# Performance work log

Hardware: AMD Instinct MI355X
Metric: run time of the kernel (lower is better)

Reference implementation:

```python
import jax, jax.numpy as jnp
import numpy as np

INPUT_DIM = 3
NUM_LEVELS = 16
LEVEL_DIM = 2
PER_LEVEL_SCALE = 2
BASE_RES = 16
MAX_PARAMS = 2 ** 19
BATCH = 2 ** 21

PRIMES = np.array([1, 2654435761, 805459861], dtype=np.uint32)
SORTED_BIN_MASK = np.triu(np.ones((INPUT_DIM + 1, INPUT_DIM), dtype=np.int32))


def _offsets():
    offs, off = [], 0
    for i in range(NUM_LEVELS):
        res = int(np.ceil(BASE_RES * PER_LEVEL_SCALE ** i))
        p = min(MAX_PARAMS, res ** INPUT_DIM)
        p = int(np.ceil(p / 32) * 32)
        off += p
        offs.append(off)
    return offs

OFFSETS = _offsets()  # cumulative, last entry = total table rows = 7114752


def setup_inputs() -> dict:
    key = jax.random.key(0)
    k1, k2 = jax.random.split(key)
    inputs = jax.random.uniform(k1, (BATCH, INPUT_DIM), dtype=jnp.float32)
    # xavier-uniform-ish init for the hash table
    total = OFFSETS[-1]
    a = float(np.sqrt(6.0 / (total + LEVEL_DIM)))
    embeddings = jax.random.uniform(k2, (total, LEVEL_DIM), dtype=jnp.float32,
                                    minval=-a, maxval=a)
    return {"inputs": inputs, "embeddings": embeddings}


def _fast_hash(ind_u32, hash_size):
    # ind_u32: [..., 3] uint32; uint32 multiply wraps mod 2^32 == (& 0xFFFFFFFF)
    h = ind_u32 * jnp.asarray(PRIMES)
    h = h[..., 0] ^ h[..., 1] ^ h[..., 2]
    return h % jnp.uint32(hash_size)


def _forward(inputs, embeddings):
    bin_mask_tbl = jnp.asarray(SORTED_BIN_MASK)  # [d+1, d]
    outs = []
    prev = 0
    for i in range(NUM_LEVELS):
        res = int(np.ceil(BASE_RES * PER_LEVEL_SCALE ** i))
        x = inputs * res                      # [B, d]
        xi = x.astype(jnp.int32)              # trunc == floor for x >= 0
        xf = x - jax.lax.stop_gradient(xi.astype(x.dtype))
        inds = jnp.argsort(xf, axis=-1)
        sorted_xf = jnp.take_along_axis(xf, inds, axis=-1)
        inv_inds = jnp.argsort(inds, axis=-1)
        bin_mask = bin_mask_tbl[:, inv_inds].transpose(1, 0, 2)  # [B, d+1, d]
        neigs = xi[:, None, :] + bin_mask                        # [B, d+1, d]
        hash_size = OFFSETS[i] - prev
        hids = _fast_hash(neigs.astype(jnp.uint32), hash_size).astype(jnp.int32) + prev
        feats = embeddings[hids]              # [B, d+1, level_dim] irregular gather
        # barycentric-style weights: consecutive diffs of sorted fracs padded with 0/1
        w_upper = jnp.concatenate([sorted_xf, jnp.ones_like(sorted_xf[..., :1])], axis=-1)
        w_lower = jnp.concatenate([jnp.zeros_like(sorted_xf[..., :1]), sorted_xf], axis=-1)
        w = (w_upper - w_lower)[..., None]    # [B, d+1, 1]
        outs.append(jnp.sum(feats * w, axis=-2))  # [B, level_dim]
        prev = OFFSETS[i]
    return jnp.concatenate(outs, axis=-1)     # [B, num_levels * level_dim]


def reference(inputs, embeddings):
    return _forward(inputs, embeddings)
```

## Files before the change

kernel.cpp:

```cpp
#include <hip/hip_runtime.h>
#include <hip/hip_fp16.h>
#include <stdint.h>


constexpr uint32_t kBatch   = 1u << 21;
constexpr size_t   kWsNeed  = (size_t)kBatch * 16u * sizeof(uint32_t);

typedef float f32x2 __attribute__((ext_vector_type(2)));
typedef float f32x4 __attribute__((ext_vector_type(4)));

constexpr uint32_t PREV[16] = {
    0u, 4096u, 36864u, 299008u, 823296u, 1347584u, 1871872u, 2396160u,
    2920448u, 3444736u, 3969024u, 4493312u, 5017600u, 5541888u, 6066176u, 6590464u};
constexpr uint32_t MASK[16] = {
    4095u, 32767u, 262143u, 524287u, 524287u, 524287u, 524287u, 524287u,
    524287u, 524287u, 524287u, 524287u, 524287u, 524287u, 524287u, 524287u};

__device__ __forceinline__ void corner_hashes_weights(
    float x0, float x1, float x2, float res, uint32_t mask, uint32_t prev,
    uint32_t& g0, uint32_t& g1, uint32_t& g2, uint32_t& g3,
    float& sa, float& sb, float& sc)
{
    const float fx0 = x0 * res;
    const float fx1 = x1 * res;
    const float fx2 = x2 * res;
    const int i0 = (int)fx0;
    const int i1 = (int)fx1;
    const int i2 = (int)fx2;
    const float f0 = fx0 - (float)i0;
    const float f1 = fx1 - (float)i1;
    const float f2 = fx2 - (float)i2;

    const int r0 = (int)(f1 < f0) + (int)(f2 < f0);
    const int r1 = (int)(f0 < f1) + (int)(f2 < f1) + (int)(f0 == f1);
    const int r2 = (int)(f0 < f2) + (int)(f1 < f2) + (int)(f0 == f2) + (int)(f1 == f2);

    sa = fminf(fminf(f0, f1), f2);
    sc = fmaxf(fmaxf(f0, f1), f2);
    sb = __builtin_amdgcn_fmed3f(f0, f1, f2);

    const uint32_t A0 = (uint32_t)i0;
    const uint32_t A1 = A0 + 1u;
    const uint32_t B0 = (uint32_t)i1 * 2654435761u;
    const uint32_t B1 = ((uint32_t)i1 + 1u) * 2654435761u;
    const uint32_t C0 = (uint32_t)i2 * 805459861u;
    const uint32_t C1 = ((uint32_t)i2 + 1u) * 805459861u;

    const uint32_t h0 = A1 ^ B1 ^ C1;
    const uint32_t h1 = (r0 >= 1 ? A1 : A0) ^ (r1 >= 1 ? B1 : B0) ^ (r2 >= 1 ? C1 : C0);
    const uint32_t h2 = (r0 >= 2 ? A1 : A0) ^ (r1 >= 2 ? B1 : B0) ^ (r2 >= 2 ? C1 : C0);
    const uint32_t h3 = A0 ^ B0 ^ C0;

    g0 = (h0 & mask) + prev;
    g1 = (h1 & mask) + prev;
    g2 = (h2 & mask) + prev;
    g3 = (h3 & mask) + prev;
}

__device__ __forceinline__ uint32_t pack_f16x2(float x, float y) {
    const __half hx = __float2half(x);
    const __half hy = __float2half(y);
    return (uint32_t)__half_as_ushort(hx) | ((uint32_t)__half_as_ushort(hy) << 16);
}

__device__ __forceinline__ float lo_h(uint32_t p) {
    return __half2float(__ushort_as_half((unsigned short)(p & 0xFFFFu)));
}
__device__ __forceinline__ float hi_h(uint32_t p) {
    return __half2float(__ushort_as_half((unsigned short)(p >> 16)));
}


__global__ __launch_bounds__(1024) void hybrid012(
    const float* __restrict__ in,
    const float* __restrict__ emb,
    uint32_t* __restrict__ scr)
{
    __shared__ uint32_t t0[4096];
    __shared__ uint32_t t1[32768];

    const uint32_t t = threadIdx.x;

#pragma unroll
    for (uint32_t i = 0u; i < 4u; ++i) {
        const uint32_t r = t + 1024u * i;
        const f32x2 v = *reinterpret_cast<const f32x2*>(emb + 2u * r);
        t0[r] = pack_f16x2(v.x, v.y);
    }
#pragma unroll
    for (uint32_t i = 0u; i < 32u; ++i) {
        const uint32_t r = t + 1024u * i;
        const f32x2 v = *reinterpret_cast<const f32x2*>(emb + 2u * (4096u + r));
        t1[r] = pack_f16x2(v.x, v.y);
    }
    __syncthreads();

    const uint32_t tid = blockIdx.x * 1024u + t;

#pragma unroll 1
    for (uint32_t k = 0u; k < 8u; ++k) {
        const uint32_t b = tid + k * 262144u;
        const float x0 = __builtin_nontemporal_load(in + 3u * b + 0u);
        const float x1 = __builtin_nontemporal_load(in + 3u * b + 1u);
        const float x2 = __builtin_nontemporal_load(in + 3u * b + 2u);

        uint32_t g0, g1, g2, g3;
        float sa2, sb2, sc2;
        corner_hashes_weights(x0, x1, x2, 64.0f, 262143u, 36864u,
                              g0, g1, g2, g3, sa2, sb2, sc2);
        f32x2 e2a = *reinterpret_cast<const f32x2*>(emb + 2u * g0);
        f32x2 e2b = *reinterpret_cast<const f32x2*>(emb + 2u * g1);
        f32x2 e2c = *reinterpret_cast<const f32x2*>(emb + 2u * g2);
        f32x2 e2d = *reinterpret_cast<const f32x2*>(emb + 2u * g3);

        {
            uint32_t l0, l1, l2, l3;
            float sa, sb, sc;
            corner_hashes_weights(x0, x1, x2, 16.0f, 4095u, 0u,
                                  l0, l1, l2, l3, sa, sb, sc);
            const uint32_t p0 = t0[l0], p1 = t0[l1], p2 = t0[l2], p3 = t0[l3];
            const float w0 = sa, w1 = sb - sa, w2 = sc - sb, w3 = 1.0f - sc;
            const float vx = w0 * lo_h(p0) + w1 * lo_h(p1) + w2 * lo_h(p2) + w3 * lo_h(p3);
            const float vy = w0 * hi_h(p0) + w1 * hi_h(p1) + w2 * hi_h(p2) + w3 * hi_h(p3);
            __builtin_nontemporal_store(pack_f16x2(vx, vy), scr + b);
        }
        {
            uint32_t l0, l1, l2, l3;
            float sa, sb, sc;
            corner_hashes_weights(x0, x1, x2, 32.0f, 32767u, 0u,
                                  l0, l1, l2, l3, sa, sb, sc);
            const uint32_t p0 = t1[l0], p1 = t1[l1], p2 = t1[l2], p3 = t1[l3];
            const float w0 = sa, w1 = sb - sa, w2 = sc - sb, w3 = 1.0f - sc;
            const float vx = w0 * lo_h(p0) + w1 * lo_h(p1) + w2 * lo_h(p2) + w3 * lo_h(p3);
            const float vy = w0 * hi_h(p0) + w1 * hi_h(p1) + w2 * hi_h(p2) + w3 * hi_h(p3);
            __builtin_nontemporal_store(pack_f16x2(vx, vy), scr + (size_t)kBatch + b);
        }

        asm volatile("" : "+v"(e2a), "+v"(e2b), "+v"(e2c), "+v"(e2d));
        const float w0 = sa2, w1 = sb2 - sa2, w2 = sc2 - sb2, w3 = 1.0f - sc2;
        const float vx = w0 * e2a.x + w1 * e2b.x + w2 * e2c.x + w3 * e2d.x;
        const float vy = w0 * e2a.y + w1 * e2b.y + w2 * e2c.y + w3 * e2d.y;
        __builtin_nontemporal_store(pack_f16x2(vx, vy), scr + (size_t)2u * kBatch + b);
    }
}


__global__ __launch_bounds__(256) void gather13(
    const float* __restrict__ in,
    const float* __restrict__ emb,
    uint32_t* __restrict__ scr)
{
    const uint32_t bid  = blockIdx.x;
    const uint32_t lvl  = 3u + (bid >> 11);
    const uint32_t tid  = (bid & 2047u) * 256u + threadIdx.x;
    const uint32_t quarter = kBatch / 4u;

    const float res = (float)(16u << lvl);
    const uint32_t mask = MASK[lvl];
    const uint32_t prev = PREV[lvl];
    uint32_t* slab = scr + (size_t)lvl * kBatch;

    f32x2 e[4][4];
    float sa[4], sb[4], sc[4];

#pragma unroll
    for (int k = 0; k < 4; ++k) {
        const uint32_t b = tid + (uint32_t)k * quarter;
        const float x0 = __builtin_nontemporal_load(in + 3u * b + 0u);
        const float x1 = __builtin_nontemporal_load(in + 3u * b + 1u);
        const float x2 = __builtin_nontemporal_load(in + 3u * b + 2u);
        uint32_t g0, g1, g2, g3;
        corner_hashes_weights(x0, x1, x2, res, mask, prev, g0, g1, g2, g3,
                              sa[k], sb[k], sc[k]);
        e[k][0] = *reinterpret_cast<const f32x2*>(emb + 2u * g0);
        e[k][1] = *reinterpret_cast<const f32x2*>(emb + 2u * g1);
        e[k][2] = *reinterpret_cast<const f32x2*>(emb + 2u * g2);
        e[k][3] = *reinterpret_cast<const f32x2*>(emb + 2u * g3);
    }

    asm volatile(""
        : "+v"(e[0][0]), "+v"(e[0][1]), "+v"(e[0][2]), "+v"(e[0][3]),
          "+v"(e[1][0]), "+v"(e[1][1]), "+v"(e[1][2]), "+v"(e[1][3]),
          "+v"(e[2][0]), "+v"(e[2][1]), "+v"(e[2][2]), "+v"(e[2][3]),
          "+v"(e[3][0]), "+v"(e[3][1]), "+v"(e[3][2]), "+v"(e[3][3]));

#pragma unroll
    for (int k = 0; k < 4; ++k) {
        const float w0 = sa[k];
        const float w1 = sb[k] - sa[k];
        const float w2 = sc[k] - sb[k];
        const float w3 = 1.0f - sc[k];
        const float vx = w0 * e[k][0].x + w1 * e[k][1].x + w2 * e[k][2].x + w3 * e[k][3].x;
        const float vy = w0 * e[k][0].y + w1 * e[k][1].y + w2 * e[k][2].y + w3 * e[k][3].y;
        const uint32_t b = tid + (uint32_t)k * quarter;
        __builtin_nontemporal_store(pack_f16x2(vx, vy), slab + b);
    }
}

__global__ __launch_bounds__(256) void transpose16(
    const uint32_t* __restrict__ scr,
    float* __restrict__ out)
{
    const uint32_t b = blockIdx.x * 256u + threadIdx.x;

    uint32_t p[16];
#pragma unroll
    for (int l = 0; l < 16; ++l)
        p[l] = __builtin_nontemporal_load(scr + (size_t)l * kBatch + b);

    float* o = out + (size_t)b * 32u;
#pragma unroll
    for (int q = 0; q < 8; ++q) {
        f32x4 t;
        t.x = lo_h(p[2 * q + 0]);
        t.y = hi_h(p[2 * q + 0]);
        t.z = lo_h(p[2 * q + 1]);
        t.w = hi_h(p[2 * q + 1]);
        *reinterpret_cast<f32x4*>(o + 4 * q) = t;
    }
}


__global__ __launch_bounds__(256) void pyramid_fwd_mono(
    const float* __restrict__ in,
    const float* __restrict__ emb,
    float* __restrict__ out)
{
    const uint32_t b = blockIdx.x * 256u + threadIdx.x;
    const float x0 = in[3u * b + 0u];
    const float x1 = in[3u * b + 1u];
    const float x2 = in[3u * b + 2u];

#pragma unroll
    for (int g = 0; g < 2; ++g) {
        float o8[16];
#pragma unroll
        for (int k = 0; k < 8; ++k) {
            const int lvl = g * 8 + k;
            const float res = (float)(16 << lvl);
            uint32_t g0, g1, g2, g3;
            float sa, sb, sc;
            corner_hashes_weights(x0, x1, x2, res, MASK[lvl], PREV[lvl],
                                  g0, g1, g2, g3, sa, sb, sc);
            const f32x2 e0 = *reinterpret_cast<const f32x2*>(emb + 2u * g0);
            const f32x2 e1 = *reinterpret_cast<const f32x2*>(emb + 2u * g1);
            const f32x2 e2 = *reinterpret_cast<const f32x2*>(emb + 2u * g2);
            const f32x2 e3 = *reinterpret_cast<const f32x2*>(emb + 2u * g3);
            const float w0 = sa, w1 = sb - sa, w2 = sc - sb, w3 = 1.0f - sc;
            o8[2 * k + 0] = w0 * e0.x + w1 * e1.x + w2 * e2.x + w3 * e3.x;
            o8[2 * k + 1] = w0 * e0.y + w1 * e1.y + w2 * e2.y + w3 * e3.y;
        }
        f32x4* o = reinterpret_cast<f32x4*>(out + (size_t)b * 32u + (size_t)g * 16u);
#pragma unroll
        for (int q = 0; q < 4; ++q) {
            f32x4 v;
            v.x = o8[4 * q + 0];
            v.y = o8[4 * q + 1];
            v.z = o8[4 * q + 2];
            v.w = o8[4 * q + 3];
            o[q] = v;
        }
    }
}


extern "C" void kernel_launch(void* const* d_in, const int* in_sizes, int n_in,
                              void* d_out, int out_size, void* d_ws, size_t ws_size,
                              hipStream_t stream) {
    const float* in  = (const float*)d_in[0];
    const float* emb = (const float*)d_in[1];
    float* out = (float*)d_out;

    if (ws_size >= kWsNeed) {
        uint32_t* scr = (uint32_t*)d_ws;
        hipLaunchKernelGGL(hybrid012, dim3(256u), dim3(1024u), 0, stream, in, emb, scr);
        hipLaunchKernelGGL(gather13, dim3(13u * 2048u), dim3(256u), 0, stream, in, emb, scr);
        hipLaunchKernelGGL(transpose16, dim3(kBatch / 256u), dim3(256u), 0, stream, scr, out);
    } else {
        hipLaunchKernelGGL(pyramid_fwd_mono, dim3(kBatch / 256u), dim3(256u), 0, stream,
                           in, emb, out);
    }
}
```

Before: 662.7 us.

## Merge LDS-level kernel and global gather kernel into one conveyor launch

```diff
diff --git a/kernel.cpp b/kernel.cpp
--- a/kernel.cpp
+++ b/kernel.cpp
@@ -4,6 +4,7 @@
 
 
 constexpr uint32_t kBatch   = 1u << 21;
+constexpr uint32_t kQuarter = kBatch / 4u;
 constexpr size_t   kWsNeed  = (size_t)kBatch * 16u * sizeof(uint32_t);
 
 typedef float f32x2 __attribute__((ext_vector_type(2)));
@@ -71,7 +72,7 @@
 }
 
 
-__global__ __launch_bounds__(1024) void hybrid012(
+__global__ __launch_bounds__(1024) void conveyor14(
     const float* __restrict__ in,
     const float* __restrict__ emb,
     uint32_t* __restrict__ scr)
@@ -79,121 +80,124 @@
     __shared__ uint32_t t0[4096];
     __shared__ uint32_t t1[32768];
 
-    const uint32_t t = threadIdx.x;
-
-#pragma unroll
-    for (uint32_t i = 0u; i < 4u; ++i) {
-        const uint32_t r = t + 1024u * i;
-        const f32x2 v = *reinterpret_cast<const f32x2*>(emb + 2u * r);
-        t0[r] = pack_f16x2(v.x, v.y);
-    }
-#pragma unroll
-    for (uint32_t i = 0u; i < 32u; ++i) {
-        const uint32_t r = t + 1024u * i;
-        const f32x2 v = *reinterpret_cast<const f32x2*>(emb + 2u * (4096u + r));
-        t1[r] = pack_f16x2(v.x, v.y);
-    }
-    __syncthreads();
-
-    const uint32_t tid = blockIdx.x * 1024u + t;
-
-#pragma unroll 1
-    for (uint32_t k = 0u; k < 8u; ++k) {
-        const uint32_t b = tid + k * 262144u;
-        const float x0 = __builtin_nontemporal_load(in + 3u * b + 0u);
-        const float x1 = __builtin_nontemporal_load(in + 3u * b + 1u);
-        const float x2 = __builtin_nontemporal_load(in + 3u * b + 2u);
-
-        uint32_t g0, g1, g2, g3;
-        float sa2, sb2, sc2;
-        corner_hashes_weights(x0, x1, x2, 64.0f, 262143u, 36864u,
-                              g0, g1, g2, g3, sa2, sb2, sc2);
-        f32x2 e2a = *reinterpret_cast<const f32x2*>(emb + 2u * g0);
-        f32x2 e2b = *reinterpret_cast<const f32x2*>(emb + 2u * g1);
-        f32x2 e2c = *reinterpret_cast<const f32x2*>(emb + 2u * g2);
-        f32x2 e2d = *reinterpret_cast<const f32x2*>(emb + 2u * g3);
-
-        {
-            uint32_t l0, l1, l2, l3;
-            float sa, sb, sc;
-            corner_hashes_weights(x0, x1, x2, 16.0f, 4095u, 0u,
-                                  l0, l1, l2, l3, sa, sb, sc);
-            const uint32_t p0 = t0[l0], p1 = t0[l1], p2 = t0[l2], p3 = t0[l3];
-            const float w0 = sa, w1 = sb - sa, w2 = sc - sb, w3 = 1.0f - sc;
-            const float vx = w0 * lo_h(p0) + w1 * lo_h(p1) + w2 * lo_h(p2) + w3 * lo_h(p3);
-            const float vy = w0 * hi_h(p0) + w1 * hi_h(p1) + w2 * hi_h(p2) + w3 * hi_h(p3);
-            __builtin_nontemporal_store(pack_f16x2(vx, vy), scr + b);
-        }
-        {
-            uint32_t l0, l1, l2, l3;
-            float sa, sb, sc;
-            corner_hashes_weights(x0, x1, x2, 32.0f, 32767u, 0u,
-                                  l0, l1, l2, l3, sa, sb, sc);
-            const uint32_t p0 = t1[l0], p1 = t1[l1], p2 = t1[l2], p3 = t1[l3];
-            const float w0 = sa, w1 = sb - sa, w2 = sc - sb, w3 = 1.0f - sc;
-            const float vx = w0 * lo_h(p0) + w1 * lo_h(p1) + w2 * lo_h(p2) + w3 * lo_h(p3);
-            const float vy = w0 * hi_h(p0) + w1 * hi_h(p1) + w2 * hi_h(p2) + w3 * hi_h(p3);
-            __builtin_nontemporal_store(pack_f16x2(vx, vy), scr + (size_t)kBatch + b);
-        }
-
-        asm volatile("" : "+v"(e2a), "+v"(e2b), "+v"(e2c), "+v"(e2d));
-        const float w0 = sa2, w1 = sb2 - sa2, w2 = sc2 - sb2, w3 = 1.0f - sc2;
-        const float vx = w0 * e2a.x + w1 * e2b.x + w2 * e2c.x + w3 * e2d.x;
-        const float vy = w0 * e2a.y + w1 * e2b.y + w2 * e2c.y + w3 * e2d.y;
-        __builtin_nontemporal_store(pack_f16x2(vx, vy), scr + (size_t)2u * kBatch + b);
-    }
-}
-
-
-__global__ __launch_bounds__(256) void gather13(
-    const float* __restrict__ in,
-    const float* __restrict__ emb,
-    uint32_t* __restrict__ scr)
-{
-    const uint32_t bid  = blockIdx.x;
-    const uint32_t lvl  = 3u + (bid >> 11);
-    const uint32_t tid  = (bid & 2047u) * 256u + threadIdx.x;
-    const uint32_t quarter = kBatch / 4u;
+    const uint32_t bid = blockIdx.x;
+    const uint32_t lvl = 2u + (bid >> 9);
+    const uint32_t tid = (bid & 511u) * 1024u + threadIdx.x;
 
     const float res = (float)(16u << lvl);
     const uint32_t mask = MASK[lvl];
     const uint32_t prev = PREV[lvl];
     uint32_t* slab = scr + (size_t)lvl * kBatch;
 
-    f32x2 e[4][4];
-    float sa[4], sb[4], sc[4];
-
-#pragma unroll
-    for (int k = 0; k < 4; ++k) {
-        const uint32_t b = tid + (uint32_t)k * quarter;
-        const float x0 = __builtin_nontemporal_load(in + 3u * b + 0u);
-        const float x1 = __builtin_nontemporal_load(in + 3u * b + 1u);
-        const float x2 = __builtin_nontemporal_load(in + 3u * b + 2u);
-        uint32_t g0, g1, g2, g3;
-        corner_hashes_weights(x0, x1, x2, res, mask, prev, g0, g1, g2, g3,
-                              sa[k], sb[k], sc[k]);
-        e[k][0] = *reinterpret_cast<const f32x2*>(emb + 2u * g0);
-        e[k][1] = *reinterpret_cast<const f32x2*>(emb + 2u * g1);
-        e[k][2] = *reinterpret_cast<const f32x2*>(emb + 2u * g2);
-        e[k][3] = *reinterpret_cast<const f32x2*>(emb + 2u * g3);
-    }
-
-    asm volatile(""
-        : "+v"(e[0][0]), "+v"(e[0][1]), "+v"(e[0][2]), "+v"(e[0][3]),
-          "+v"(e[1][0]), "+v"(e[1][1]), "+v"(e[1][2]), "+v"(e[1][3]),
-          "+v"(e[2][0]), "+v"(e[2][1]), "+v"(e[2][2]), "+v"(e[2][3]),
-          "+v"(e[3][0]), "+v"(e[3][1]), "+v"(e[3][2]), "+v"(e[3][3]));
-
-#pragma unroll
-    for (int k = 0; k < 4; ++k) {
-        const float w0 = sa[k];
-        const float w1 = sb[k] - sa[k];
-        const float w2 = sc[k] - sb[k];
-        const float w3 = 1.0f - sc[k];
-        const float vx = w0 * e[k][0].x + w1 * e[k][1].x + w2 * e[k][2].x + w3 * e[k][3].x;
-        const float vy = w0 * e[k][0].y + w1 * e[k][1].y + w2 * e[k][2].y + w3 * e[k][3].y;
-        const uint32_t b = tid + (uint32_t)k * quarter;
-        __builtin_nontemporal_store(pack_f16x2(vx, vy), slab + b);
+    if (lvl == 2u) {
+#pragma unroll
+        for (uint32_t i = 0u; i < 4u; ++i) {
+            const uint32_t r = threadIdx.x + 1024u * i;
+            const f32x2 v = *reinterpret_cast<const f32x2*>(emb + 2u * r);
+            t0[r] = pack_f16x2(v.x, v.y);
+        }
+#pragma unroll
+        for (uint32_t i = 0u; i < 32u; ++i) {
+            const uint32_t r = threadIdx.x + 1024u * i;
+            const f32x2 v = *reinterpret_cast<const f32x2*>(emb + 2u * (4096u + r));
+            t1[r] = pack_f16x2(v.x, v.y);
+        }
+        __syncthreads();
+
+        float xin[4][3];
+        f32x2 e[4][4];
+        float sa2[4], sb2[4], sc2[4];
+#pragma unroll
+        for (int k = 0; k < 4; ++k) {
+            const uint32_t b = tid + (uint32_t)k * kQuarter;
+            xin[k][0] = __builtin_nontemporal_load(in + 3u * b + 0u);
+            xin[k][1] = __builtin_nontemporal_load(in + 3u * b + 1u);
+            xin[k][2] = __builtin_nontemporal_load(in + 3u * b + 2u);
+            uint32_t g0, g1, g2, g3;
+            corner_hashes_weights(xin[k][0], xin[k][1], xin[k][2], res, mask, prev,
+                                  g0, g1, g2, g3, sa2[k], sb2[k], sc2[k]);
+            e[k][0] = *reinterpret_cast<const f32x2*>(emb + 2u * g0);
+            e[k][1] = *reinterpret_cast<const f32x2*>(emb + 2u * g1);
+            e[k][2] = *reinterpret_cast<const f32x2*>(emb + 2u * g2);
+            e[k][3] = *reinterpret_cast<const f32x2*>(emb + 2u * g3);
+        }
+
+#pragma unroll
+        for (int k = 0; k < 4; ++k) {
+            const uint32_t b = tid + (uint32_t)k * kQuarter;
+            {
+                uint32_t l0, l1, l2, l3;
+                float sa, sb, sc;
+                corner_hashes_weights(xin[k][0], xin[k][1], xin[k][2],
+                                      16.0f, 4095u, 0u, l0, l1, l2, l3, sa, sb, sc);
+                const uint32_t p0 = t0[l0], p1 = t0[l1], p2 = t0[l2], p3 = t0[l3];
+                const float w0 = sa, w1 = sb - sa, w2 = sc - sb, w3 = 1.0f - sc;
+                const float vx = w0 * lo_h(p0) + w1 * lo_h(p1) + w2 * lo_h(p2) + w3 * lo_h(p3);
+                const float vy = w0 * hi_h(p0) + w1 * hi_h(p1) + w2 * hi_h(p2) + w3 * hi_h(p3);
+                __builtin_nontemporal_store(pack_f16x2(vx, vy), scr + b);
+            }
+            {
+                uint32_t l0, l1, l2, l3;
+                float sa, sb, sc;
+                corner_hashes_weights(xin[k][0], xin[k][1], xin[k][2],
+                                      32.0f, 32767u, 0u, l0, l1, l2, l3, sa, sb, sc);
+                const uint32_t p0 = t1[l0], p1 = t1[l1], p2 = t1[l2], p3 = t1[l3];
+                const float w0 = sa, w1 = sb - sa, w2 = sc - sb, w3 = 1.0f - sc;
+                const float vx = w0 * lo_h(p0) + w1 * lo_h(p1) + w2 * lo_h(p2) + w3 * lo_h(p3);
+                const float vy = w0 * hi_h(p0) + w1 * hi_h(p1) + w2 * hi_h(p2) + w3 * hi_h(p3);
+                __builtin_nontemporal_store(pack_f16x2(vx, vy), scr + (size_t)kBatch + b);
+            }
+        }
+
+        asm volatile(""
+            : "+v"(e[0][0]), "+v"(e[0][1]), "+v"(e[0][2]), "+v"(e[0][3]),
+              "+v"(e[1][0]), "+v"(e[1][1]), "+v"(e[1][2]), "+v"(e[1][3]),
+              "+v"(e[2][0]), "+v"(e[2][1]), "+v"(e[2][2]), "+v"(e[2][3]),
+              "+v"(e[3][0]), "+v"(e[3][1]), "+v"(e[3][2]), "+v"(e[3][3]));
+#pragma unroll
+        for (int k = 0; k < 4; ++k) {
+            const float w0 = sa2[k];
+            const float w1 = sb2[k] - sa2[k];
+            const float w2 = sc2[k] - sb2[k];
+            const float w3 = 1.0f - sc2[k];
+            const float vx = w0 * e[k][0].x + w1 * e[k][1].x + w2 * e[k][2].x + w3 * e[k][3].x;
+            const float vy = w0 * e[k][0].y + w1 * e[k][1].y + w2 * e[k][2].y + w3 * e[k][3].y;
+            const uint32_t b = tid + (uint32_t)k * kQuarter;
+            __builtin_nontemporal_store(pack_f16x2(vx, vy), slab + b);
+        }
+    } else {
+        f32x2 e[4][4];
+        float sa[4], sb[4], sc[4];
+#pragma unroll
+        for (int k = 0; k < 4; ++k) {
+            const uint32_t b = tid + (uint32_t)k * kQuarter;
+            const float x0 = __builtin_nontemporal_load(in + 3u * b + 0u);
+            const float x1 = __builtin_nontemporal_load(in + 3u * b + 1u);
+            const float x2 = __builtin_nontemporal_load(in + 3u * b + 2u);
+            uint32_t g0, g1, g2, g3;
+            corner_hashes_weights(x0, x1, x2, res, mask, prev, g0, g1, g2, g3,
+                                  sa[k], sb[k], sc[k]);
+            e[k][0] = *reinterpret_cast<const f32x2*>(emb + 2u * g0);
+            e[k][1] = *reinterpret_cast<const f32x2*>(emb + 2u * g1);
+            e[k][2] = *reinterpret_cast<const f32x2*>(emb + 2u * g2);
+            e[k][3] = *reinterpret_cast<const f32x2*>(emb + 2u * g3);
+        }
+        asm volatile(""
+            : "+v"(e[0][0]), "+v"(e[0][1]), "+v"(e[0][2]), "+v"(e[0][3]),
+              "+v"(e[1][0]), "+v"(e[1][1]), "+v"(e[1][2]), "+v"(e[1][3]),
+              "+v"(e[2][0]), "+v"(e[2][1]), "+v"(e[2][2]), "+v"(e[2][3]),
+              "+v"(e[3][0]), "+v"(e[3][1]), "+v"(e[3][2]), "+v"(e[3][3]));
+#pragma unroll
+        for (int k = 0; k < 4; ++k) {
+            const float w0 = sa[k];
+            const float w1 = sb[k] - sa[k];
+            const float w2 = sc[k] - sb[k];
+            const float w3 = 1.0f - sc[k];
+            const float vx = w0 * e[k][0].x + w1 * e[k][1].x + w2 * e[k][2].x + w3 * e[k][3].x;
+            const float vy = w0 * e[k][0].y + w1 * e[k][1].y + w2 * e[k][2].y + w3 * e[k][3].y;
+            const uint32_t b = tid + (uint32_t)k * kQuarter;
+            __builtin_nontemporal_store(pack_f16x2(vx, vy), slab + b);
+        }
     }
 }
 
@@ -273,9 +277,10 @@
 
     if (ws_size >= kWsNeed) {
         uint32_t* scr = (uint32_t*)d_ws;
-        hipLaunchKernelGGL(hybrid012, dim3(256u), dim3(1024u), 0, stream, in, emb, scr);
-        hipLaunchKernelGGL(gather13, dim3(13u * 2048u), dim3(256u), 0, stream, in, emb, scr);
-        hipLaunchKernelGGL(transpose16, dim3(kBatch / 256u), dim3(256u), 0, stream, scr, out);
+        hipLaunchKernelGGL(conveyor14, dim3(14u * 512u), dim3(1024u), 0, stream,
+                           in, emb, scr);
+        hipLaunchKernelGGL(transpose16, dim3(kBatch / 256u), dim3(256u), 0, stream,
+                           scr, out);
     } else {
         hipLaunchKernelGGL(pyramid_fwd_mono, dim3(kBatch / 256u), dim3(256u), 0, stream,
                            in, emb, out);
```

Measured after the change: 668.8 us. About the same (+0.9%).

## Merge low-level shared-table kernel and high-level gather kernel into one launch

Applied to the files above, without the earlier changes.

```diff
diff --git a/kernel.cpp b/kernel.cpp
--- a/kernel.cpp
+++ b/kernel.cpp
@@ -4,6 +4,7 @@
 
 
 constexpr uint32_t kBatch   = 1u << 21;
+constexpr uint32_t kQuarter = kBatch / 4u;
 constexpr size_t   kWsNeed  = (size_t)kBatch * 16u * sizeof(uint32_t);
 
 typedef float f32x2 __attribute__((ext_vector_type(2)));
@@ -71,7 +72,7 @@
 }
 
 
-__global__ __launch_bounds__(1024) void hybrid012(
+__global__ __launch_bounds__(1024) void conveyor16(
     const float* __restrict__ in,
     const float* __restrict__ emb,
     uint32_t* __restrict__ scr)
@@ -79,121 +80,111 @@
     __shared__ uint32_t t0[4096];
     __shared__ uint32_t t1[32768];
 
-    const uint32_t t = threadIdx.x;
-
-#pragma unroll
-    for (uint32_t i = 0u; i < 4u; ++i) {
-        const uint32_t r = t + 1024u * i;
-        const f32x2 v = *reinterpret_cast<const f32x2*>(emb + 2u * r);
-        t0[r] = pack_f16x2(v.x, v.y);
-    }
-#pragma unroll
-    for (uint32_t i = 0u; i < 32u; ++i) {
-        const uint32_t r = t + 1024u * i;
-        const f32x2 v = *reinterpret_cast<const f32x2*>(emb + 2u * (4096u + r));
-        t1[r] = pack_f16x2(v.x, v.y);
-    }
-    __syncthreads();
-
-    const uint32_t tid = blockIdx.x * 1024u + t;
+    const uint32_t bid = blockIdx.x;
+
+    if (bid < 13u * 512u) {
+        const uint32_t lvl = 3u + (bid >> 9);
+        const uint32_t tid = (bid & 511u) * 1024u + threadIdx.x;
+
+        const float res = (float)(16u << lvl);
+        const uint32_t mask = MASK[lvl];
+        const uint32_t prev = PREV[lvl];
+        uint32_t* slab = scr + (size_t)lvl * kBatch;
+
+        f32x2 e[4][4];
+        float sa[4], sb[4], sc[4];
+#pragma unroll
+        for (int k = 0; k < 4; ++k) {
+            const uint32_t b = tid + (uint32_t)k * kQuarter;
+            const float x0 = __builtin_nontemporal_load(in + 3u * b + 0u);
+            const float x1 = __builtin_nontemporal_load(in + 3u * b + 1u);
+            const float x2 = __builtin_nontemporal_load(in + 3u * b + 2u);
+            uint32_t g0, g1, g2, g3;
+            corner_hashes_weights(x0, x1, x2, res, mask, prev, g0, g1, g2, g3,
+                                  sa[k], sb[k], sc[k]);
+            e[k][0] = *reinterpret_cast<const f32x2*>(emb + 2u * g0);
+            e[k][1] = *reinterpret_cast<const f32x2*>(emb + 2u * g1);
+            e[k][2] = *reinterpret_cast<const f32x2*>(emb + 2u * g2);
+            e[k][3] = *reinterpret_cast<const f32x2*>(emb + 2u * g3);
+        }
+        asm volatile(""
+            : "+v"(e[0][0]), "+v"(e[0][1]), "+v"(e[0][2]), "+v"(e[0][3]),
+              "+v"(e[1][0]), "+v"(e[1][1]), "+v"(e[1][2]), "+v"(e[1][3]),
+              "+v"(e[2][0]), "+v"(e[2][1]), "+v"(e[2][2]), "+v"(e[2][3]),
+              "+v"(e[3][0]), "+v"(e[3][1]), "+v"(e[3][2]), "+v"(e[3][3]));
+#pragma unroll
+        for (int k = 0; k < 4; ++k) {
+            const float w0 = sa[k];
+            const float w1 = sb[k] - sa[k];
+            const float w2 = sc[k] - sb[k];
+            const float w3 = 1.0f - sc[k];
+            const float vx = w0 * e[k][0].x + w1 * e[k][1].x + w2 * e[k][2].x + w3 * e[k][3].x;
+            const float vy = w0 * e[k][0].y + w1 * e[k][1].y + w2 * e[k][2].y + w3 * e[k][3].y;
+            const uint32_t b = tid + (uint32_t)k * kQuarter;
+            __builtin_nontemporal_store(pack_f16x2(vx, vy), slab + b);
+        }
+    } else {
+        const uint32_t htid = (bid - 13u * 512u) * 1024u + threadIdx.x;
+
+#pragma unroll
+        for (uint32_t i = 0u; i < 4u; ++i) {
+            const uint32_t r = threadIdx.x + 1024u * i;
+            const f32x2 v = *reinterpret_cast<const f32x2*>(emb + 2u * r);
+            t0[r] = pack_f16x2(v.x, v.y);
+        }
+#pragma unroll
+        for (uint32_t i = 0u; i < 32u; ++i) {
+            const uint32_t r = threadIdx.x + 1024u * i;
+            const f32x2 v = *reinterpret_cast<const f32x2*>(emb + 2u * (4096u + r));
+            t1[r] = pack_f16x2(v.x, v.y);
+        }
+        __syncthreads();
 
 #pragma unroll 1
-    for (uint32_t k = 0u; k < 8u; ++k) {
-        const uint32_t b = tid + k * 262144u;
-        const float x0 = __builtin_nontemporal_load(in + 3u * b + 0u);
-        const float x1 = __builtin_nontemporal_load(in + 3u * b + 1u);
-        const float x2 = __builtin_nontemporal_load(in + 3u * b + 2u);
-
-        uint32_t g0, g1, g2, g3;
-        float sa2, sb2, sc2;
-        corner_hashes_weights(x0, x1, x2, 64.0f, 262143u, 36864u,
-                              g0, g1, g2, g3, sa2, sb2, sc2);
-        f32x2 e2a = *reinterpret_cast<const f32x2*>(emb + 2u * g0);
-        f32x2 e2b = *reinterpret_cast<const f32x2*>(emb + 2u * g1);
-        f32x2 e2c = *reinterpret_cast<const f32x2*>(emb + 2u * g2);
-        f32x2 e2d = *reinterpret_cast<const f32x2*>(emb + 2u * g3);
-
-        {
-            uint32_t l0, l1, l2, l3;
-            float sa, sb, sc;
-            corner_hashes_weights(x0, x1, x2, 16.0f, 4095u, 0u,
-                                  l0, l1, l2, l3, sa, sb, sc);
-            const uint32_t p0 = t0[l0], p1 = t0[l1], p2 = t0[l2], p3 = t0[l3];
-            const float w0 = sa, w1 = sb - sa, w2 = sc - sb, w3 = 1.0f - sc;
-            const float vx = w0 * lo_h(p0) + w1 * lo_h(p1) + w2 * lo_h(p2) + w3 * lo_h(p3);
-            const float vy = w0 * hi_h(p0) + w1 * hi_h(p1) + w2 * hi_h(p2) + w3 * hi_h(p3);
-            __builtin_nontemporal_store(pack_f16x2(vx, vy), scr + b);
-        }
-        {
-            uint32_t l0, l1, l2, l3;
-            float sa, sb, sc;
-            corner_hashes_weights(x0, x1, x2, 32.0f, 32767u, 0u,
-                                  l0, l1, l2, l3, sa, sb, sc);
-            const uint32_t p0 = t1[l0], p1 = t1[l1], p2 = t1[l2], p3 = t1[l3];
-            const float w0 = sa, w1 = sb - sa, w2 = sc - sb, w3 = 1.0f - sc;
-            const float vx = w0 * lo_h(p0) + w1 * lo_h(p1) + w2 * lo_h(p2) + w3 * lo_h(p3);
-            const float vy = w0 * hi_h(p0) + w1 * hi_h(p1) + w2 * hi_h(p2) + w3 * hi_h(p3);
-            __builtin_nontemporal_store(pack_f16x2(vx, vy), scr + (size_t)kBatch + b);
-        }
-
-        asm volatile("" : "+v"(e2a), "+v"(e2b), "+v"(e2c), "+v"(e2d));
-        const float w0 = sa2, w1 = sb2 - sa2, w2 = sc2 - sb2, w3 = 1.0f - sc2;
-        const float vx = w0 * e2a.x + w1 * e2b.x + w2 * e2c.x + w3 * e2d.x;
-        const float vy = w0 * e2a.y + w1 * e2b.y + w2 * e2c.y + w3 * e2d.y;
-        __builtin_nontemporal_store(pack_f16x2(vx, vy), scr + (size_t)2u * kBatch + b);
-    }
-}
-
-
-__global__ __launch_bounds__(256) void gather13(
-    const float* __restrict__ in,
-    const float* __restrict__ emb,
-    uint32_t* __restrict__ scr)
-{
-    const uint32_t bid  = blockIdx.x;
-    const uint32_t lvl  = 3u + (bid >> 11);
-    const uint32_t tid  = (bid & 2047u) * 256u + threadIdx.x;
-    const uint32_t quarter = kBatch / 4u;
-
-    const float res = (float)(16u << lvl);
-    const uint32_t mask = MASK[lvl];
-    const uint32_t prev = PREV[lvl];
-    uint32_t* slab = scr + (size_t)lvl * kBatch;
-
-    f32x2 e[4][4];
-    float sa[4], sb[4], sc[4];
-
-#pragma unroll
-    for (int k = 0; k < 4; ++k) {
-        const uint32_t b = tid + (uint32_t)k * quarter;
-        const float x0 = __builtin_nontemporal_load(in + 3u * b + 0u);
-        const float x1 = __builtin_nontemporal_load(in + 3u * b + 1u);
-        const float x2 = __builtin_nontemporal_load(in + 3u * b + 2u);
-        uint32_t g0, g1, g2, g3;
-        corner_hashes_weights(x0, x1, x2, res, mask, prev, g0, g1, g2, g3,
-                              sa[k], sb[k], sc[k]);
-        e[k][0] = *reinterpret_cast<const f32x2*>(emb + 2u * g0);
-        e[k][1] = *reinterpret_cast<const f32x2*>(emb + 2u * g1);
-        e[k][2] = *reinterpret_cast<const f32x2*>(emb + 2u * g2);
-        e[k][3] = *reinterpret_cast<const f32x2*>(emb + 2u * g3);
-    }
-
-    asm volatile(""
-        : "+v"(e[0][0]), "+v"(e[0][1]), "+v"(e[0][2]), "+v"(e[0][3]),
-          "+v"(e[1][0]), "+v"(e[1][1]), "+v"(e[1][2]), "+v"(e[1][3]),
-          "+v"(e[2][0]), "+v"(e[2][1]), "+v"(e[2][2]), "+v"(e[2][3]),
-          "+v"(e[3][0]), "+v"(e[3][1]), "+v"(e[3][2]), "+v"(e[3][3]));
-
-#pragma unroll
-    for (int k = 0; k < 4; ++k) {
-        const float w0 = sa[k];
-        const float w1 = sb[k] - sa[k];
-        const float w2 = sc[k] - sb[k];
-        const float w3 = 1.0f - sc[k];
-        const float vx = w0 * e[k][0].x + w1 * e[k][1].x + w2 * e[k][2].x + w3 * e[k][3].x;
-        const float vy = w0 * e[k][0].y + w1 * e[k][1].y + w2 * e[k][2].y + w3 * e[k][3].y;
-        const uint32_t b = tid + (uint32_t)k * quarter;
-        __builtin_nontemporal_store(pack_f16x2(vx, vy), slab + b);
+        for (uint32_t k = 0u; k < 8u; ++k) {
+            const uint32_t b = htid + k * 262144u;
+            const float x0 = __builtin_nontemporal_load(in + 3u * b + 0u);
+            const float x1 = __builtin_nontemporal_load(in + 3u * b + 1u);
+            const float x2 = __builtin_nontemporal_load(in + 3u * b + 2u);
+
+            uint32_t g0, g1, g2, g3;
+            float sa2, sb2, sc2;
+            corner_hashes_weights(x0, x1, x2, 64.0f, 262143u, 36864u,
+                                  g0, g1, g2, g3, sa2, sb2, sc2);
+            f32x2 e2a = *reinterpret_cast<const f32x2*>(emb + 2u * g0);
+            f32x2 e2b = *reinterpret_cast<const f32x2*>(emb + 2u * g1);
+            f32x2 e2c = *reinterpret_cast<const f32x2*>(emb + 2u * g2);
+            f32x2 e2d = *reinterpret_cast<const f32x2*>(emb + 2u * g3);
+
+            {
+                uint32_t l0, l1, l2, l3;
+                float sa, sb, sc;
+                corner_hashes_weights(x0, x1, x2, 16.0f, 4095u, 0u,
+                                      l0, l1, l2, l3, sa, sb, sc);
+                const uint32_t p0 = t0[l0], p1 = t0[l1], p2 = t0[l2], p3 = t0[l3];
+                const float w0 = sa, w1 = sb - sa, w2 = sc - sb, w3 = 1.0f - sc;
+                const float vx = w0 * lo_h(p0) + w1 * lo_h(p1) + w2 * lo_h(p2) + w3 * lo_h(p3);
+                const float vy = w0 * hi_h(p0) + w1 * hi_h(p1) + w2 * hi_h(p2) + w3 * hi_h(p3);
+                __builtin_nontemporal_store(pack_f16x2(vx, vy), scr + b);
+            }
+            {
+                uint32_t l0, l1, l2, l3;
+                float sa, sb, sc;
+                corner_hashes_weights(x0, x1, x2, 32.0f, 32767u, 0u,
+                                      l0, l1, l2, l3, sa, sb, sc);
+                const uint32_t p0 = t1[l0], p1 = t1[l1], p2 = t1[l2], p3 = t1[l3];
+                const float w0 = sa, w1 = sb - sa, w2 = sc - sb, w3 = 1.0f - sc;
+                const float vx = w0 * lo_h(p0) + w1 * lo_h(p1) + w2 * lo_h(p2) + w3 * lo_h(p3);
+                const float vy = w0 * hi_h(p0) + w1 * hi_h(p1) + w2 * hi_h(p2) + w3 * hi_h(p3);
+                __builtin_nontemporal_store(pack_f16x2(vx, vy), scr + (size_t)kBatch + b);
+            }
+
+            asm volatile("" : "+v"(e2a), "+v"(e2b), "+v"(e2c), "+v"(e2d));
+            const float w0 = sa2, w1 = sb2 - sa2, w2 = sc2 - sb2, w3 = 1.0f - sc2;
+            const float vx = w0 * e2a.x + w1 * e2b.x + w2 * e2c.x + w3 * e2d.x;
+            const float vy = w0 * e2a.y + w1 * e2b.y + w2 * e2c.y + w3 * e2d.y;
+            __builtin_nontemporal_store(pack_f16x2(vx, vy), scr + (size_t)2u * kBatch + b);
+        }
     }
 }
 
@@ -273,9 +264,10 @@
 
     if (ws_size >= kWsNeed) {
         uint32_t* scr = (uint32_t*)d_ws;
-        hipLaunchKernelGGL(hybrid012, dim3(256u), dim3(1024u), 0, stream, in, emb, scr);
-        hipLaunchKernelGGL(gather13, dim3(13u * 2048u), dim3(256u), 0, stream, in, emb, scr);
-        hipLaunchKernelGGL(transpose16, dim3(kBatch / 256u), dim3(256u), 0, stream, scr, out);
+        hipLaunchKernelGGL(conveyor16, dim3(13u * 512u + 256u), dim3(1024u), 0, stream,
+                           in, emb, scr);
+        hipLaunchKernelGGL(transpose16, dim3(kBatch / 256u), dim3(256u), 0, stream,
+                           scr, out);
     } else {
         hipLaunchKernelGGL(pyramid_fwd_mono, dim3(kBatch / 256u), dim3(256u), 0, stream,
                            in, emb, out);
```

Result: slower. 678.4 us (+2.4%).
